# Performance work log

Measured on AMD Instinct MI355X. Metric: run time of the kernel, lower is better.

## Reference

```python
import jax, jax.numpy as jnp
import numpy as np

B, T, D, H, O = 256, 512, 256, 512, 1


def setup_inputs() -> dict:
    key = jax.random.key(0)
    ks = jax.random.split(key, 4)
    x = jax.random.normal(ks[0], (B, T, D), dtype=jnp.float32)
    W = jax.random.normal(ks[1], (D, 3 * H), dtype=jnp.float32) * (1.0 / np.sqrt(D))
    U = jax.random.normal(ks[2], (H, 3 * H), dtype=jnp.float32) * (1.0 / np.sqrt(H))
    b = jnp.zeros((3 * H,), dtype=jnp.float32)
    Wd = jax.random.normal(ks[3], (H, O), dtype=jnp.float32) * (1.0 / np.sqrt(H))
    bd = jnp.zeros((O,), dtype=jnp.float32)
    return {"x": x, "W": W, "U": U, "b": b, "Wd": Wd, "bd": bd}


def _gru_last_hidden(x, W, U, b):
    # x: [B, T, D]; returns final hidden state [B, H]
    units = U.shape[0]
    bz, br, bn = b[:units], b[units:2 * units], b[2 * units:]
    Uzr, Un = U[:, :2 * units], U[:, 2 * units:]
    # precompute input projections for all timesteps: [B, T, 3H] -> [T, B, 3H]
    gx = jnp.einsum('btd,dk->tbk', x, W)

    def step(h, gx_t):
        gxz = gx_t[:, :units]
        gxr = gx_t[:, units:2 * units]
        gxn = gx_t[:, 2 * units:]
        gh_zr = h @ Uzr                      # [B, 2H]
        z = jax.nn.sigmoid(gxz + gh_zr[:, :units] + bz)
        r = jax.nn.sigmoid(gxr + gh_zr[:, units:] + br)
        n = jnp.tanh(gxn + (r * h) @ Un + bn)
        h_new = z * h + (1.0 - z) * n
        return h_new, None

    h0 = jnp.zeros((x.shape[0], units), dtype=x.dtype)
    h_last, _ = jax.lax.scan(step, h0, gx)
    return h_last


def reference(x, W, U, b, Wd, bd):
    h_last = _gru_last_hidden(x, W, U, b)  # [B, H]
    return h_last @ Wd + bd                # [B, O]
```

## Files before the change

kernel.cpp:

```cpp
#include <hip/hip_runtime.h>
#include <hip/hip_bf16.h>

typedef __attribute__((ext_vector_type(8))) short short8;
typedef __attribute__((ext_vector_type(4))) float f32x4;
typedef __attribute__((ext_vector_type(4))) unsigned int u32x4;
typedef __attribute__((ext_vector_type(4))) unsigned short u16x4;

#define T_STEPS 512
#define DIM_D 256
#define DIM_H 512
#define NGROUP 8
#define NCOL 32
#define BB 32
#define SLC 16
#define FSTRIDE 32
#define MAXP 16384

__device__ __forceinline__ unsigned short f2bf(float f) {
  union { float f; unsigned u; } v; v.f = f;
  unsigned r = v.u + 0x7fffu + ((v.u >> 16) & 1u);
  return (unsigned short)(r >> 16);
}
__device__ __forceinline__ float sigm(float x) { return 1.0f / (1.0f + __expf(-x)); }
__device__ __forceinline__ float tanh_fast(float x) { return 2.0f / (1.0f + __expf(-2.0f * x)) - 1.0f; }

__device__ __forceinline__ void ldg8_bypass(const void* p, u32x4* o) {
  asm volatile(
      "global_load_dwordx4 %0, %8, off sc0 sc1\n\t"
      "global_load_dwordx4 %1, %8, off offset:16 sc0 sc1\n\t"
      "global_load_dwordx4 %2, %8, off offset:32 sc0 sc1\n\t"
      "global_load_dwordx4 %3, %8, off offset:48 sc0 sc1\n\t"
      "global_load_dwordx4 %4, %8, off offset:64 sc0 sc1\n\t"
      "global_load_dwordx4 %5, %8, off offset:80 sc0 sc1\n\t"
      "global_load_dwordx4 %6, %8, off offset:96 sc0 sc1\n\t"
      "global_load_dwordx4 %7, %8, off offset:112 sc0 sc1\n\t"
      "s_waitcnt vmcnt(0)"
      : "=&v"(o[0]), "=&v"(o[1]), "=&v"(o[2]), "=&v"(o[3]),
        "=&v"(o[4]), "=&v"(o[5]), "=&v"(o[6]), "=&v"(o[7])
      : "v"(p)
      : "memory");
}
__device__ __forceinline__ void atom_st_u32(unsigned* p, unsigned v) {
  asm volatile("global_atomic_swap %0, %1, off" :: "v"(p), "v"(v) : "memory");
}

__global__ void k_init(unsigned* hx_u32, unsigned* flags) {
  int i = blockIdx.x * 256 + threadIdx.x;
  if (i < 65536) hx_u32[i] = 0u;
  if (i < 2 * NGROUP * 64 * FSTRIDE) flags[i] = 0u;
}

__global__ void k_packW(const float* __restrict__ W, unsigned short* __restrict__ Wt) {
  int n = blockIdx.x, k = threadIdx.x;
  Wt[n * 256 + k] = f2bf(W[(size_t)k * 1536 + n]);
}

__global__ void k_packU(const float* __restrict__ U, unsigned short* __restrict__ Ut) {
  int n = blockIdx.x;
  for (int k = threadIdx.x; k < 512; k += 256)
    Ut[n * 512 + k] = f2bf(U[(size_t)k * 1536 + n]);
}

__global__ void k_out(const float* __restrict__ part, const float* __restrict__ bd,
                      float* __restrict__ out) {
  int b = threadIdx.x;
  float s = bd[0];
  for (int c = 0; c < 32; c++) s += part[c * 256 + b];
  out[b] = s;
}

__global__ void __launch_bounds__(256, 1)
k_gru(const float* __restrict__ x, const float* __restrict__ bias,
      const float* __restrict__ Wd,
      const unsigned short* __restrict__ Wt, const unsigned short* __restrict__ Ut,
      unsigned short* hx, unsigned short* rhx,
      float* part, unsigned* flags) {
  extern __shared__ char smem[];
  char* sUzr = smem;
  char* sUn  = smem + 32768;
  char* sW   = smem + 49152;
  char* sH   = smem + 73728;
  char* sX   = smem + 106496;
  float* sHM = (float*)(smem + 122880);

  const int tid = threadIdx.x;
  const int bid = blockIdx.x;
  const int g = bid & 7;
  const int c = bid >> 3;
  const int w = tid >> 6;
  const int l = tid & 63;
  const int lrow = l & 15;
  const int lk = l >> 4;
  const int n0 = c * SLC;
  const int mt = w & 1;
  const bool zw = (w < 2);

  unsigned* fA = flags + g * 64 * FSTRIDE;
  unsigned* fB = flags + NGROUP * 64 * FSTRIDE + g * 64 * FSTRIDE;

  unsigned short* hx_g  = hx  + (size_t)g * (BB * DIM_H);
  unsigned short* rhx_g = rhx + (size_t)g * (BB * DIM_H);
  unsigned* hx32_g  = (unsigned*)hx_g;
  unsigned* rhx32_g = (unsigned*)rhx_g;

  for (int q = tid; q < 2048; q += 256) {
    int n = q >> 6, ch = q & 63;
    int grow = (n < 16) ? (n0 + n) : (DIM_H + n0 + (n - 16));
    u32x4 v = *(const u32x4*)(Ut + (size_t)grow * DIM_H + ch * 8);
    *(u32x4*)(sUzr + n * 1024 + ((ch * 16) ^ ((n & 7) << 4))) = v;
  }
  for (int q = tid; q < 1024; q += 256) {
    int n = q >> 6, ch = q & 63;
    int grow = 2 * DIM_H + n0 + n;
    u32x4 v = *(const u32x4*)(Ut + (size_t)grow * DIM_H + ch * 8);
    *(u32x4*)(sUn + n * 1024 + ((ch * 16) ^ ((n & 7) << 4))) = v;
  }
  for (int q = tid; q < 1536; q += 256) {
    int n = q >> 5, ch = q & 31;
    int grow = (n < 16) ? (n0 + n) : (n < 32 ? (DIM_H + n0 + (n - 16))
                                             : (2 * DIM_H + n0 + (n - 32)));
    u32x4 v = *(const u32x4*)(Wt + (size_t)grow * DIM_D + ch * 8);
    *(u32x4*)(sW + n * 512 + ((ch * 16) ^ ((n & 7) << 4))) = v;
  }
  sHM[tid] = 0.0f; sHM[tid + 256] = 0.0f;
  const float bz_l = bias[n0 + lrow];
  const float br_l = bias[DIM_H + n0 + lrow];
  const float bn_l = bias[2 * DIM_H + n0 + lrow];
  __syncthreads();

  f32x4 azr, an;

  auto stage_x = [&](int t) {
    const int xr = tid >> 3;
    const int xj = (tid & 7) * 32;
    const float* xp = x + ((size_t)(g * BB + xr) * T_STEPS + t) * DIM_D + xj;
#pragma unroll
    for (int i = 0; i < 8; i++) {
      float4 v = ((const float4*)xp)[i];
      u16x4 h4 = { f2bf(v.x), f2bf(v.y), f2bf(v.z), f2bf(v.w) };
      int kb = (xj + i * 4) * 2;
      *(u16x4*)(sX + xr * 512 + (kb ^ ((xr & 7) << 4))) = h4;
    }
  };

  auto w_mfma = [&]() {
    float bini = zw ? bz_l : br_l;
    f32x4 t0 = { bini, bini, bini, bini };
    azr = t0;
    f32x4 t1 = { bn_l, bn_l, bn_l, bn_l };
    an = t1;
    const int arow = mt * 16 + lrow;
    const int nzr = zw ? lrow : (16 + lrow);
    const int nnn = 32 + lrow;
#pragma unroll
    for (int ks = 0; ks < 8; ks++) {
      int kb = ks * 64 + lk * 16;
      short8 a = *(const short8*)(sX + arow * 512 + (kb ^ ((arow & 7) << 4)));
      short8 b0 = *(const short8*)(sW + nzr * 512 + (kb ^ ((nzr & 7) << 4)));
      azr = __builtin_amdgcn_mfma_f32_16x16x32_bf16(a, b0, azr, 0, 0, 0);
      if (zw) {
        short8 b1 = *(const short8*)(sW + nnn * 512 + (kb ^ ((nnn & 7) << 4)));
        an = __builtin_amdgcn_mfma_f32_16x16x32_bf16(a, b1, an, 0, 0, 0);
      }
    }
  };

  auto pollload = [&](const unsigned short* src_base, unsigned* f, unsigned e) {
    const int hr = tid >> 3;
    const int ck = tid & 7;
    const int half = hr >> 4;
    const unsigned* fp = f + (((unsigned)(ck << 3)) | half) * FSTRIDE;
    for (int it = 0; it < MAXP; ++it) {
      unsigned a0, a1, a2, a3;
      asm volatile(
          "global_load_dword %0, %4, off sc0 sc1\n\t"
          "global_load_dword %1, %4, off offset:256 sc0 sc1\n\t"
          "global_load_dword %2, %4, off offset:512 sc0 sc1\n\t"
          "global_load_dword %3, %4, off offset:768 sc0 sc1\n\t"
          "s_waitcnt vmcnt(0)"
          : "=&v"(a0), "=&v"(a1), "=&v"(a2), "=&v"(a3)
          : "v"(fp)
          : "memory");
      if (a0 >= e && a1 >= e && a2 >= e && a3 >= e) break;
      __builtin_amdgcn_s_sleep(1);
    }
    const char* s0 = (const char*)(src_base + hr * DIM_H) + ck * 128;
    u32x4 v[8];
    ldg8_bypass(s0, v);
    char* dst = sH + hr * 1024;
    const int sw = (hr & 7) << 4;
#pragma unroll
    for (int i = 0; i < 8; i++)
      *(u32x4*)(dst + ((ck * 128 + i * 16) ^ sw)) = v[i];
  };

  auto uzr_mfma = [&]() {
    const int arow = mt * 16 + lrow;
    const int n = zw ? lrow : (16 + lrow);
#pragma unroll
    for (int ks = 0; ks < 16; ks++) {
      int kb = ks * 64 + lk * 16;
      short8 a = *(const short8*)(sH + arow * 1024 + (kb ^ ((arow & 7) << 4)));
      short8 b8 = *(const short8*)(sUzr + n * 1024 + (kb ^ ((n & 7) << 4)));
      azr = __builtin_amdgcn_mfma_f32_16x16x32_bf16(a, b8, azr, 0, 0, 0);
    }
  };

  auto un_mfma = [&]() {
    const int arow = mt * 16 + lrow;
#pragma unroll
    for (int ks = 0; ks < 16; ks++) {
      int kb = ks * 64 + lk * 16;
      short8 a = *(const short8*)(sH + arow * 1024 + (kb ^ ((arow & 7) << 4)));
      short8 b8 = *(const short8*)(sUn + lrow * 1024 + (kb ^ ((lrow & 7) << 4)));
      an = __builtin_amdgcn_mfma_f32_16x16x32_bf16(a, b8, an, 0, 0, 0);
    }
  };

  stage_x(0);
  __syncthreads();
  w_mfma();

  for (int t = 0; t < T_STEPS; t++) {
    const unsigned e1 = (unsigned)(t + 1);

    pollload(hx_g, fB, (unsigned)t);
    __syncthreads();
    uzr_mfma();
    if (!zw) {
#pragma unroll
      for (int j = 0; j < 4; j++) {
        int row = mt * 16 + lk * 4 + j;
        float rv = sigm(azr[j]);
        unsigned mv = (unsigned)f2bf(rv * sHM[row * 16 + lrow]);
        unsigned nb = (unsigned)__shfl_xor((int)mv, 1, 64) & 0xFFFFu;
        if (!(lrow & 1))
          atom_st_u32(rhx32_g + row * 256 + ((n0 + lrow) >> 1), mv | (nb << 16));
      }
    }
    __syncthreads();
    if (!zw) {
      asm volatile("s_waitcnt vmcnt(0)" ::: "memory");
      if (l == 0) atom_st_u32(fA + ((c << 1) | mt) * FSTRIDE, e1);
    }

    pollload(rhx_g, fA, e1);
    __syncthreads();
    if (zw) {
      un_mfma();
#pragma unroll
      for (int j = 0; j < 4; j++) {
        int row = mt * 16 + lk * 4 + j;
        float zv = sigm(azr[j]);
        float nv = tanh_fast(an[j]);
        float hv = sHM[row * 16 + lrow];
        float hn = zv * hv + (1.0f - zv) * nv;
        sHM[row * 16 + lrow] = hn;
        if (t + 1 < T_STEPS) {
          unsigned mv = (unsigned)f2bf(hn);
          unsigned nb = (unsigned)__shfl_xor((int)mv, 1, 64) & 0xFFFFu;
          if (!(lrow & 1))
            atom_st_u32(hx32_g + row * 256 + ((n0 + lrow) >> 1), mv | (nb << 16));
        }
      }
    }
    if (t + 1 < T_STEPS) stage_x(t + 1);
    if (zw && t + 1 < T_STEPS) {
      asm volatile("s_waitcnt vmcnt(0)" ::: "memory");
      if (l == 0) atom_st_u32(fB + ((c << 1) | mt) * FSTRIDE, e1);
    }
    __syncthreads();
    if (t + 1 < T_STEPS) w_mfma();
  }

  if (tid < BB) {
    float s = 0.0f;
#pragma unroll
    for (int i = 0; i < SLC; i++) s += sHM[tid * 16 + i] * Wd[n0 + i];
    part[c * 256 + g * BB + tid] = s;
  }
}

extern "C" void kernel_launch(void* const* d_in, const int* in_sizes, int n_in,
                              void* d_out, int out_size, void* d_ws, size_t ws_size,
                              hipStream_t stream) {
  const float* x    = (const float*)d_in[0];
  const float* W    = (const float*)d_in[1];
  const float* U    = (const float*)d_in[2];
  const float* bias = (const float*)d_in[3];
  const float* Wd   = (const float*)d_in[4];
  const float* bd   = (const float*)d_in[5];
  float* out = (float*)d_out;
  char* ws = (char*)d_ws;

  unsigned short* Wt  = (unsigned short*)(ws + 0);
  unsigned short* Ut  = (unsigned short*)(ws + 786432);
  unsigned short* hx  = (unsigned short*)(ws + 2359296);
  unsigned short* rhx = (unsigned short*)(ws + 2621440);
  float* part         = (float*)(ws + 2883584);
  unsigned* flags     = (unsigned*)(ws + 2916352);

  hipFuncSetAttribute((const void*)k_gru, hipFuncAttributeMaxDynamicSharedMemorySize, 124928);

  k_init<<<256, 256, 0, stream>>>((unsigned*)hx, flags);
  k_packW<<<1536, 256, 0, stream>>>(W, Wt);
  k_packU<<<1536, 256, 0, stream>>>(U, Ut);
  k_gru<<<256, 256, 124928, stream>>>(x, bias, Wd, Wt, Ut, hx, rhx, part, flags);
  k_out<<<1, 256, 0, stream>>>(part, bd, out);
}
```

Before: 4.958 ms.

## Replace workgroup barriers after hidden-state staging with per-chunk LDS counters

Each thread bumps a shared-memory counter for its K-chunk after staging its slice of the hidden state, in place of a block-wide barrier. Consumer waves spin on each chunk's counter and start MFMAs on early chunks while later chunks are still loading. This aims to overlap the polling and global loads with compute inside each recurrent step. It adds LDS atomics and spin loops, and the poll cap is raised.

```diff
diff --git a/kernel.cpp b/kernel.cpp
--- a/kernel.cpp
+++ b/kernel.cpp
@@ -14,7 +14,7 @@
 #define BB 32
 #define SLC 16
 #define FSTRIDE 32
-#define MAXP 16384
+#define MAXP 20000
 
 __device__ __forceinline__ unsigned short f2bf(float f) {
   union { float f; unsigned u; } v; v.f = f;
@@ -82,6 +82,7 @@
   char* sH   = smem + 73728;
   char* sX   = smem + 106496;
   float* sHM = (float*)(smem + 122880);
+  unsigned* sCnt = (unsigned*)(smem + 124928);
 
   const int tid = threadIdx.x;
   const int bid = blockIdx.x;
@@ -123,6 +124,7 @@
     *(u32x4*)(sW + n * 512 + ((ch * 16) ^ ((n & 7) << 4))) = v;
   }
   sHM[tid] = 0.0f; sHM[tid + 256] = 0.0f;
+  if (tid < 8) sCnt[tid] = 0u;
   const float bz_l = bias[n0 + lrow];
   const float br_l = bias[DIM_H + n0 + lrow];
   const float bn_l = bias[2 * DIM_H + n0 + lrow];
@@ -165,7 +167,7 @@
     }
   };
 
-  auto pollload = [&](const unsigned short* src_base, unsigned* f, unsigned e) {
+  auto pollstage = [&](const unsigned short* src_base, unsigned* f, unsigned e, int ph) {
     const int hr = tid >> 3;
     const int ck = tid & 7;
     const int half = hr >> 4;
@@ -192,13 +194,24 @@
 #pragma unroll
     for (int i = 0; i < 8; i++)
       *(u32x4*)(dst + ((ck * 128 + i * 16) ^ sw)) = v[i];
-  };
-
-  auto uzr_mfma = [&]() {
+    __hip_atomic_fetch_add(sCnt + ph * 4 + (ck >> 1), 1u,
+                           __ATOMIC_RELEASE, __HIP_MEMORY_SCOPE_WORKGROUP);
+  };
+
+  auto chunk_spin = [&](int ph, int k, unsigned tgt) {
+    volatile unsigned* cp = sCnt + ph * 4 + k;
+    for (int it = 0; it < (1 << 20); ++it) {
+      if (*cp >= tgt) break;
+      __builtin_amdgcn_s_sleep(1);
+    }
+    asm volatile("" ::: "memory");
+  };
+
+  auto uzr_chunk = [&](int k) {
     const int arow = mt * 16 + lrow;
     const int n = zw ? lrow : (16 + lrow);
 #pragma unroll
-    for (int ks = 0; ks < 16; ks++) {
+    for (int ks = 4 * k; ks < 4 * k + 4; ks++) {
       int kb = ks * 64 + lk * 16;
       short8 a = *(const short8*)(sH + arow * 1024 + (kb ^ ((arow & 7) << 4)));
       short8 b8 = *(const short8*)(sUzr + n * 1024 + (kb ^ ((n & 7) << 4)));
@@ -206,10 +219,10 @@
     }
   };
 
-  auto un_mfma = [&]() {
+  auto un_chunk = [&](int k) {
     const int arow = mt * 16 + lrow;
 #pragma unroll
-    for (int ks = 0; ks < 16; ks++) {
+    for (int ks = 4 * k; ks < 4 * k + 4; ks++) {
       int kb = ks * 64 + lk * 16;
       short8 a = *(const short8*)(sH + arow * 1024 + (kb ^ ((arow & 7) << 4)));
       short8 b8 = *(const short8*)(sUn + lrow * 1024 + (kb ^ ((lrow & 7) << 4)));
@@ -223,10 +236,10 @@
 
   for (int t = 0; t < T_STEPS; t++) {
     const unsigned e1 = (unsigned)(t + 1);
-
-    pollload(hx_g, fB, (unsigned)t);
-    __syncthreads();
-    uzr_mfma();
+    const unsigned tgt = 64u * e1;
+
+    pollstage(hx_g, fB, (unsigned)t, 0);
+    for (int k = 0; k < 4; k++) { chunk_spin(0, k, tgt); uzr_chunk(k); }
     if (!zw) {
 #pragma unroll
       for (int j = 0; j < 4; j++) {
@@ -244,10 +257,9 @@
       if (l == 0) atom_st_u32(fA + ((c << 1) | mt) * FSTRIDE, e1);
     }
 
-    pollload(rhx_g, fA, e1);
-    __syncthreads();
+    pollstage(rhx_g, fA, e1, 1);
     if (zw) {
-      un_mfma();
+      for (int k = 0; k < 4; k++) { chunk_spin(1, k, tgt); un_chunk(k); }
 #pragma unroll
       for (int j = 0; j < 4; j++) {
         int row = mt * 16 + lk * 4 + j;
@@ -300,11 +312,11 @@
   float* part         = (float*)(ws + 2883584);
   unsigned* flags     = (unsigned*)(ws + 2916352);
 
-  hipFuncSetAttribute((const void*)k_gru, hipFuncAttributeMaxDynamicSharedMemorySize, 124928);
+  hipFuncSetAttribute((const void*)k_gru, hipFuncAttributeMaxDynamicSharedMemorySize, 124992);
 
   k_init<<<256, 256, 0, stream>>>((unsigned*)hx, flags);
   k_packW<<<1536, 256, 0, stream>>>(W, Wt);
   k_packU<<<1536, 256, 0, stream>>>(U, Ut);
-  k_gru<<<256, 256, 124928, stream>>>(x, bias, Wd, Wt, Ut, hx, rhx, part, flags);
+  k_gru<<<256, 256, 124992, stream>>>(x, bias, Wd, Wt, Ut, hx, rhx, part, flags);
   k_out<<<1, 256, 0, stream>>>(part, bd, out);
 }
```

New measurement: 5.536 ms. 1.12x slower.
